# Optimization experiments

Hardware: AMD Instinct MI355X
Metric: run time of the kernel (lower is better)

The kernel has to match this reference:

```python
import jax, jax.numpy as jnp
import numpy as np

C_IN = 256   # c_m
C_H = 32     # outer_product_dim
C_Z = 128
B, S, N = 1, 128, 256  # batch, msa depth, n_res
EPS = 1e-5


def setup_inputs() -> dict:
    key = jax.random.key(0)
    ks = jax.random.split(key, 10)
    msa = jax.random.normal(ks[0], (B, S, N, C_IN), dtype=jnp.float32)
    mask = jax.random.uniform(ks[1], (B, S, N), dtype=jnp.float32)
    ln_w = jnp.ones((C_IN,), jnp.float32)
    ln_b = jnp.zeros((C_IN,), jnp.float32)
    # weights stored [in, out] (torch Linear transposed)
    wl = jax.random.normal(ks[2], (C_IN, C_H), jnp.float32) / np.sqrt(C_IN)
    bl = jnp.zeros((C_H,), jnp.float32)
    wr = jax.random.normal(ks[3], (C_IN, C_H), jnp.float32) / np.sqrt(C_IN)
    br = jnp.zeros((C_H,), jnp.float32)
    wo = jax.random.normal(ks[4], (C_H * C_H, C_Z), jnp.float32) / np.sqrt(C_H * C_H)
    bo = jnp.zeros((C_Z,), jnp.float32)
    return {"msa_representation": msa, "msa_mask": mask, "ln_w": ln_w, "ln_b": ln_b,
            "wl": wl, "bl": bl, "wr": wr, "br": br, "wo": wo, "bo": bo}


def _layer_norm(x, w, b):
    mu = jnp.mean(x, axis=-1, keepdims=True)
    var = jnp.var(x, axis=-1, keepdims=True)
    return (x - mu) * jax.lax.rsqrt(var + EPS) * w + b


def reference(msa_representation, msa_mask, ln_w, ln_b, wl, bl, wr, br, wo, bo):
    x = _layer_norm(msa_representation, ln_w, ln_b)            # [b,s,i,c_in]
    A = x @ wl + bl                                            # [b,s,i,c]
    Bm = x @ wr + br                                           # [b,s,j,d]
    m = msa_mask
    A = A * m[..., None]
    Bm = Bm * m[..., None]
    outer = jnp.einsum('bsic,bsjd->bijcd', A, Bm)              # [b,i,j,c,d]
    norm = jnp.clip(jnp.einsum('bsi,bsj->bij', m, m), 1.0, None)
    mean_val = outer / norm[..., None, None]
    b_, i_, j_ = mean_val.shape[:3]
    mean_val = mean_val.reshape(b_, i_, j_, -1)                # [b,i,j,c*d]
    return mean_val @ wo + bo                                  # [b,i,j,c_z]
```

## Files before the change

kernel.cpp:

```cpp
#include <hip/hip_runtime.h>
#include <hip/hip_bf16.h>
#include <stdint.h>

#define SDEP 128
#define NRES 256
#define CZQ 128

typedef __bf16 v8bf __attribute__((ext_vector_type(8)));
typedef __bf16 v4bf __attribute__((ext_vector_type(4)));
typedef float v16f __attribute__((ext_vector_type(16)));

__device__ __forceinline__ float dpp_wave_sum(float x) {
  float t;
#define STEP(ctrl)                                                         \
  t = __builtin_bit_cast(float, __builtin_amdgcn_update_dpp(               \
          0, __builtin_bit_cast(int, x), ctrl, 0xF, 0xF, true));           \
  x += t;
  STEP(0x111)
  STEP(0x112)
  STEP(0x114)
  STEP(0x118)
  STEP(0x142)
  STEP(0x143)
#undef STEP
  return x;
}
__device__ __forceinline__ float lane63(float x) {
  return __builtin_bit_cast(float,
      __builtin_amdgcn_readlane(__builtin_bit_cast(int, x), 63));
}

__global__ __launch_bounds__(512, 2) void fusedA_kernel(
    const float* __restrict__ msa, const float* __restrict__ lnw,
    const float* __restrict__ lnb, const float* __restrict__ wl,
    const float* __restrict__ wr, const float* __restrict__ mask,
    const float* __restrict__ wo, const float* __restrict__ bl,
    const float* __restrict__ br,
    __bf16* __restrict__ At2, __bf16* __restrict__ Bt2,
    float* __restrict__ rnorm, __bf16* __restrict__ wot4)
{
  __shared__ __bf16 xs[128 * 258];
  __shared__ __bf16 wcs[16384];
  __shared__ __bf16 Ls[8 * 32 * 36];

  const int i = blockIdx.x, t = threadIdx.x;
  const int w = t >> 6, lane = t & 63;
  const int half = lane >> 5, l31 = lane & 31;
  const int sb = w >> 1, nh = w & 1;

  #pragma unroll
  for (int u = 0; u < 32; ++u) {
    int idx = u * 512 + t;
    int j = idx & 7, n = (idx >> 3) & 31, hf = (idx >> 8) & 1;
    int ks = (idx >> 9) & 15, tile = idx >> 13;
    const float* wsrc = tile ? wr : wl;
    wcs[idx] = (__bf16)wsrc[(ks * 16 + hf * 8 + j) * 32 + n];
  }

  const float4 wv4 = ((const float4*)lnw)[lane];
  const float4 bv4 = ((const float4*)lnb)[lane];

  #pragma unroll 8
  for (int r = 0; r < 16; ++r) {
    const int s = sb * 32 + nh * 16 + r;
    float4 x = ((const float4*)(msa + ((size_t)s * 256 + i) * 256))[lane];
    float s1 = dpp_wave_sum(x.x + x.y + x.z + x.w);
    float s2 = dpp_wave_sum(x.x * x.x + x.y * x.y + x.z * x.z + x.w * x.w);
    float mu = lane63(s1) * (1.f / 256.f);
    float var = lane63(s2) * (1.f / 256.f) - mu * mu;
    float rs = rsqrtf(var + 1e-5f);
    v4bf o;
    o[0] = (__bf16)((x.x - mu) * rs * wv4.x + bv4.x);
    o[1] = (__bf16)((x.y - mu) * rs * wv4.y + bv4.y);
    o[2] = (__bf16)((x.z - mu) * rs * wv4.z + bv4.z);
    o[3] = (__bf16)((x.w - mu) * rs * wv4.w + bv4.w);
    *(v4bf*)(xs + s * 258 + lane * 4) = o;
  }
  __syncthreads();

  v16f acc;
  #pragma unroll
  for (int r = 0; r < 16; ++r) acc[r] = 0.f;

  const __bf16* xrow = xs + (sb * 32 + l31) * 258 + half * 8;
  const __bf16* bbase = wcs + nh * 8192 + half * 256 + l31 * 8;
  #pragma unroll
  for (int ks = 0; ks < 16; ++ks) {
    v8bf a = *(const v8bf*)(xrow + ks * 16);
    v8bf b = *(const v8bf*)(bbase + ks * 512);
    acc = __builtin_amdgcn_mfma_f32_32x32x16_bf16(a, b, acc, 0, 0, 0);
  }

  __bf16* Lw = Ls + w * 32 * 36;
  const float bias = (nh ? br : bl)[l31];
  #pragma unroll
  for (int r = 0; r < 16; ++r) {
    int sl = (r & 3) + 8 * (r >> 2) + 4 * half;
    float mv = mask[(sb * 32 + sl) * NRES + i];
    Lw[l31 * 36 + sl] = (__bf16)((acc[r] + bias) * mv);
  }

  __bf16* dst = nh ? Bt2 : At2;
  const int c = lane >> 1, jq = (lane & 1) * 4;
  #pragma unroll
  for (int o = 0; o < 4; ++o) {
    v4bf v = *(const v4bf*)(Lw + c * 36 + o * 8 + jq);
    *(v4bf*)(dst + ((size_t)i * 16 + sb * 4 + o) * 256 + lane * 4) = v;
  }

  if (i < 128) {
    const int b = i * 2 + (t >> 8), col = t & 255;
    float a0 = 0.f;
    #pragma unroll 4
    for (int s = 0; s < SDEP; ++s)
      a0 += mask[s * NRES + b] * mask[s * NRES + col];
    rnorm[b * NRES + col] = 1.f / fmaxf(a0, 1.f);
  } else {
    #pragma unroll
    for (int u = 0; u < 2; ++u) {
      int idx = (i - 128) * 1024 + u * 512 + t;
      int j = idx & 7, lc = (idx >> 3) & 63, kk = (idx >> 9) & 63, zg = idx >> 15;
      int k = kk * 16 + (lc >> 5) * 8 + j;
      int z = zg * 32 + (lc & 31);
      wot4[idx] = (__bf16)wo[k * CZQ + z];
    }
  }
}

__global__ __launch_bounds__(512, 4) void outer_kernel(
    const __bf16* __restrict__ At2, const __bf16* __restrict__ Bt2,
    const float* __restrict__ rnorm, const __bf16* __restrict__ wot4,
    const float* __restrict__ bo, float* __restrict__ out)
{
  __shared__ char smem[74240];
  __bf16* Ps   = (__bf16*)smem;
  __bf16* redb = (__bf16*)(smem + 66048);

  const int tid = threadIdx.x;
  const int w = tid >> 6, lane = tid & 63;
  const int half = lane >> 5, l31 = lane & 31;
  const int bx = blockIdx.x;
  const int by = blockIdx.y;
  const int mh = w >> 2;
  const int nq = w & 3;

  const __bf16* Ap = At2 + ((size_t)(by * 4 + mh * 2)) * 4096 + l31 * 8;
  const __bf16* Bp = Bt2 + ((size_t)(bx * 8 + nq * 2)) * 4096 + l31 * 8;

  v16f acc[2][2];
  #pragma unroll
  for (int a = 0; a < 2; ++a)
    #pragma unroll
    for (int b = 0; b < 2; ++b)
      #pragma unroll
      for (int r = 0; r < 16; ++r) acc[a][b][r] = 0.f;

  #pragma unroll
  for (int ks = 0; ks < 8; ++ks) {
    const int off = (ks * 2 + half) * 256;
    v8bf a0 = *(const v8bf*)(Ap + off);
    v8bf a1 = *(const v8bf*)(Ap + 4096 + off);
    v8bf b0 = *(const v8bf*)(Bp + off);
    v8bf b1 = *(const v8bf*)(Bp + 4096 + off);
    acc[0][0] = __builtin_amdgcn_mfma_f32_32x32x16_bf16(a0, b0, acc[0][0], 0, 0, 0);
    acc[0][1] = __builtin_amdgcn_mfma_f32_32x32x16_bf16(a0, b1, acc[0][1], 0, 0, 0);
    acc[1][0] = __builtin_amdgcn_mfma_f32_32x32x16_bf16(a1, b0, acc[1][0], 0, 0, 0);
    acc[1][1] = __builtin_amdgcn_mfma_f32_32x32x16_bf16(a1, b1, acc[1][1], 0, 0, 0);
  }

  #pragma unroll
  for (int ti = 0; ti < 2; ++ti) {
    #pragma unroll
    for (int tj = 0; tj < 2; ++tj) {
      const int it = mh * 2 + ti, jt = nq * 2 + tj;
      const int p = it * 8 + jt;
      const float rn = rnorm[(by * 4 + it) * NRES + bx * 8 + jt];
      #pragma unroll
      for (int r = 0; r < 16; ++r) {
        int cc = (r & 3) + 8 * (r >> 2) + 4 * half;
        Ps[p * 1032 + cc * 32 + l31] = (__bf16)(acc[ti][tj][r] * rn);
      }
    }
  }

  const int zg = w & 3, kh = w >> 2;
  const __bf16* wp = wot4 + ((size_t)((zg * 64 + kh * 32) * 64) + half * 32 + l31) * 8;
  v8bf wb[8];
  #pragma unroll
  for (int u = 0; u < 8; ++u)
    wb[u] = *(const v8bf*)(wp + u * 512);

  __syncthreads();

  const __bf16* pp = Ps + l31 * 1032 + kh * 512 + half * 8;

  v16f c2;
  #pragma unroll
  for (int r = 0; r < 16; ++r) c2[r] = 0.f;

  #pragma unroll
  for (int g = 0; g < 4; ++g) {
    #pragma unroll
    for (int u = 0; u < 8; ++u) {
      const int kk = g * 8 + u;
      v8bf bb = wb[u];
      if (g < 3) wb[u] = *(const v8bf*)(wp + (kk + 8) * 512);
      v8bf aa = *(const v8bf*)(pp + kk * 16);
      c2 = __builtin_amdgcn_mfma_f32_32x32x16_bf16(aa, bb, c2, 0, 0, 0);
    }
  }

  if (kh == 1) {
    #pragma unroll
    for (int r = 0; r < 16; ++r) {
      int cc = (r & 3) + 8 * (r >> 2) + 4 * half;
      redb[zg * 1024 + cc * 32 + l31] = (__bf16)c2[r];
    }
  }
  __syncthreads();

  if (kh == 0) {
    const float bz = bo[zg * 32 + l31];
    #pragma unroll
    for (int r = 0; r < 16; ++r) {
      int cc = (r & 3) + 8 * (r >> 2) + 4 * half;
      float v = c2[r] + (float)redb[zg * 1024 + cc * 32 + l31] + bz;
      int i = by * 4 + (cc >> 3), j = bx * 8 + (cc & 7);
      out[((size_t)i * NRES + j) * CZQ + zg * 32 + l31] = v;
    }
  }
}

extern "C" void kernel_launch(void* const* d_in, const int* in_sizes, int n_in,
                              void* d_out, int out_size, void* d_ws, size_t ws_size,
                              hipStream_t stream) {
  const float* msa  = (const float*)d_in[0];
  const float* mask = (const float*)d_in[1];
  const float* lnw  = (const float*)d_in[2];
  const float* lnb  = (const float*)d_in[3];
  const float* wl   = (const float*)d_in[4];
  const float* bl   = (const float*)d_in[5];
  const float* wr   = (const float*)d_in[6];
  const float* br   = (const float*)d_in[7];
  const float* wo   = (const float*)d_in[8];
  const float* bo   = (const float*)d_in[9];
  float* out = (float*)d_out;

  char* ws = (char*)d_ws;
  __bf16* At2   = (__bf16*)(ws);
  __bf16* Bt2   = (__bf16*)(ws + 2097152);
  float*  rnorm = (float*)(ws + 4194304);
  __bf16* wot4  = (__bf16*)(ws + 4456448);

  fusedA_kernel<<<256, 512, 0, stream>>>(msa, lnw, lnb, wl, wr, mask, wo,
                                         bl, br, At2, Bt2, rnorm, wot4);
  outer_kernel<<<dim3(32, 64), 512, 0, stream>>>(At2, Bt2, rnorm, wot4, bo, out);
}
```

Measured before the change: 150.3 us.

## Make outer kernel persistent over 8 tiles with software-pipelined double-buffered stages

The outer-product kernel now launches 256 blocks instead of 2048, and each block loops over 8 consecutive j-tiles. Inside each iteration the first GEMM for the next tile is interleaved with the projection GEMM of the current tile, with Ps and redb double-buffered in shared memory. Half of the wo tile stays resident in registers for the whole block. The aim is to hide global-load and MFMA latency and amortize weight loading across tiles. In exchange it uses more registers and shared memory, occupancy drops to 2 blocks per CU, and only 256 blocks may leave CUs idle.

```diff
diff --git a/kernel.cpp b/kernel.cpp
--- a/kernel.cpp
+++ b/kernel.cpp
@@ -29,6 +29,8 @@
   return __builtin_bit_cast(float,
       __builtin_amdgcn_readlane(__builtin_bit_cast(int, x), 63));
 }
+
+#define MFMA32(a, b, c) __builtin_amdgcn_mfma_f32_32x32x16_bf16(a, b, c, 0, 0, 0)
 
 __global__ __launch_bounds__(512, 2) void fusedA_kernel(
     const float* __restrict__ msa, const float* __restrict__ lnw,
@@ -88,7 +90,7 @@
   for (int ks = 0; ks < 16; ++ks) {
     v8bf a = *(const v8bf*)(xrow + ks * 16);
     v8bf b = *(const v8bf*)(bbase + ks * 512);
-    acc = __builtin_amdgcn_mfma_f32_32x32x16_bf16(a, b, acc, 0, 0, 0);
+    acc = MFMA32(a, b, acc);
   }
 
   __bf16* Lw = Ls + w * 32 * 36;
@@ -127,106 +129,172 @@
   }
 }
 
-__global__ __launch_bounds__(512, 4) void outer_kernel(
+__global__ __launch_bounds__(512, 2) void outer_kernel(
     const __bf16* __restrict__ At2, const __bf16* __restrict__ Bt2,
     const float* __restrict__ rnorm, const __bf16* __restrict__ wot4,
     const float* __restrict__ bo, float* __restrict__ out)
 {
-  __shared__ char smem[74240];
-  __bf16* Ps   = (__bf16*)smem;
-  __bf16* redb = (__bf16*)(smem + 66048);
+  __shared__ __bf16 Ps[2][32 * 1032];
+  __shared__ __bf16 redb[2][4 * 1024];
 
   const int tid = threadIdx.x;
   const int w = tid >> 6, lane = tid & 63;
   const int half = lane >> 5, l31 = lane & 31;
-  const int bx = blockIdx.x;
-  const int by = blockIdx.y;
-  const int mh = w >> 2;
-  const int nq = w & 3;
+  const int bid = blockIdx.x;
+  const int by = bid >> 2;
+  const int bxg = (bid & 3) * 8;
+  const int mh = w >> 2, nq = w & 3;
+  const int zg = w & 3, kh = w >> 2;
+
+  const __bf16* wp =
+      wot4 + ((size_t)((zg * 64 + kh * 32) * 64) + half * 32 + l31) * 8;
+  v8bf wbr[16];
+  #pragma unroll
+  for (int u = 0; u < 16; ++u) wbr[u] = *(const v8bf*)(wp + u * 512);
 
   const __bf16* Ap = At2 + ((size_t)(by * 4 + mh * 2)) * 4096 + l31 * 8;
-  const __bf16* Bp = Bt2 + ((size_t)(bx * 8 + nq * 2)) * 4096 + l31 * 8;
 
   v16f acc[2][2];
-  #pragma unroll
-  for (int a = 0; a < 2; ++a)
-    #pragma unroll
-    for (int b = 0; b < 2; ++b)
-      #pragma unroll
-      for (int r = 0; r < 16; ++r) acc[a][b][r] = 0.f;
-
-  #pragma unroll
-  for (int ks = 0; ks < 8; ++ks) {
-    const int off = (ks * 2 + half) * 256;
-    v8bf a0 = *(const v8bf*)(Ap + off);
-    v8bf a1 = *(const v8bf*)(Ap + 4096 + off);
-    v8bf b0 = *(const v8bf*)(Bp + off);
-    v8bf b1 = *(const v8bf*)(Bp + 4096 + off);
-    acc[0][0] = __builtin_amdgcn_mfma_f32_32x32x16_bf16(a0, b0, acc[0][0], 0, 0, 0);
-    acc[0][1] = __builtin_amdgcn_mfma_f32_32x32x16_bf16(a0, b1, acc[0][1], 0, 0, 0);
-    acc[1][0] = __builtin_amdgcn_mfma_f32_32x32x16_bf16(a1, b0, acc[1][0], 0, 0, 0);
-    acc[1][1] = __builtin_amdgcn_mfma_f32_32x32x16_bf16(a1, b1, acc[1][1], 0, 0, 0);
-  }
-
-  #pragma unroll
-  for (int ti = 0; ti < 2; ++ti) {
-    #pragma unroll
-    for (int tj = 0; tj < 2; ++tj) {
-      const int it = mh * 2 + ti, jt = nq * 2 + tj;
-      const int p = it * 8 + jt;
-      const float rn = rnorm[(by * 4 + it) * NRES + bx * 8 + jt];
+
+  {
+    const __bf16* Bp = Bt2 + ((size_t)(bxg * 8 + nq * 2)) * 4096 + l31 * 8;
+    #pragma unroll
+    for (int a = 0; a < 2; ++a)
+      #pragma unroll
+      for (int b = 0; b < 2; ++b)
+        #pragma unroll
+        for (int r = 0; r < 16; ++r) acc[a][b][r] = 0.f;
+    #pragma unroll
+    for (int ks = 0; ks < 8; ++ks) {
+      const int off = (ks * 2 + half) * 256;
+      v8bf a0 = *(const v8bf*)(Ap + off);
+      v8bf a1 = *(const v8bf*)(Ap + 4096 + off);
+      v8bf b0 = *(const v8bf*)(Bp + off);
+      v8bf b1 = *(const v8bf*)(Bp + 4096 + off);
+      acc[0][0] = MFMA32(a0, b0, acc[0][0]);
+      acc[0][1] = MFMA32(a0, b1, acc[0][1]);
+      acc[1][0] = MFMA32(a1, b0, acc[1][0]);
+      acc[1][1] = MFMA32(a1, b1, acc[1][1]);
+    }
+    #pragma unroll
+    for (int ti = 0; ti < 2; ++ti) {
+      #pragma unroll
+      for (int tj = 0; tj < 2; ++tj) {
+        const int it = mh * 2 + ti, jt = nq * 2 + tj;
+        const int p = it * 8 + jt;
+        const float rn = rnorm[(by * 4 + it) * NRES + bxg * 8 + jt];
+        #pragma unroll
+        for (int r = 0; r < 16; ++r) {
+          int cc = (r & 3) + 8 * (r >> 2) + 4 * half;
+          Ps[0][p * 1032 + cc * 32 + l31] = (__bf16)(acc[ti][tj][r] * rn);
+        }
+      }
+    }
+  }
+  __syncthreads();
+
+  const __bf16* pp0 = &Ps[0][l31 * 1032 + kh * 512 + half * 8];
+  const __bf16* pp1 = &Ps[1][l31 * 1032 + kh * 512 + half * 8];
+  const float bz = bo[zg * 32 + l31];
+
+  #pragma unroll 1
+  for (int t = 0; t < 8; ++t) {
+    const int pb = t & 1;
+    const int bxn = (t < 7) ? (bxg + t + 1) : bxg;
+    const __bf16* Bp = Bt2 + ((size_t)(bxn * 8 + nq * 2)) * 4096 + l31 * 8;
+    const __bf16* pp = pb ? pp1 : pp0;
+
+    float rn[2][2];
+    #pragma unroll
+    for (int ti = 0; ti < 2; ++ti)
+      #pragma unroll
+      for (int tj = 0; tj < 2; ++tj)
+        rn[ti][tj] =
+            rnorm[(by * 4 + mh * 2 + ti) * NRES + bxn * 8 + nq * 2 + tj];
+
+    #pragma unroll
+    for (int a = 0; a < 2; ++a)
+      #pragma unroll
+      for (int b = 0; b < 2; ++b)
+        #pragma unroll
+        for (int r = 0; r < 16; ++r) acc[a][b][r] = 0.f;
+
+    v16f c2;
+    #pragma unroll
+    for (int r = 0; r < 16; ++r) c2[r] = 0.f;
+
+    v8bf la[2][4];
+    v8bf ws[8];
+
+    {
+      const int off = half * 256;
+      la[0][0] = *(const v8bf*)(Ap + off);
+      la[0][1] = *(const v8bf*)(Ap + 4096 + off);
+      la[0][2] = *(const v8bf*)(Bp + off);
+      la[0][3] = *(const v8bf*)(Bp + 4096 + off);
+    }
+
+    #pragma unroll
+    for (int kk = 0; kk < 32; ++kk) {
+      v8bf aa = *(const v8bf*)(pp + kk * 16);
+      v8bf bb;
+      if (kk < 16) bb = wbr[kk];
+      else         bb = ws[(kk - 16) & 7];
+      c2 = MFMA32(aa, bb, c2);
+
+      if (kk >= 8 && kk < 24)
+        ws[(kk - 8) & 7] = *(const v8bf*)(wp + (kk + 8) * 512);
+
+      if ((kk & 3) == 0 && kk < 28) {
+        const int g = (kk >> 2) + 1;
+        const int off = (g * 2 + half) * 256;
+        la[g & 1][0] = *(const v8bf*)(Ap + off);
+        la[g & 1][1] = *(const v8bf*)(Ap + 4096 + off);
+        la[g & 1][2] = *(const v8bf*)(Bp + off);
+        la[g & 1][3] = *(const v8bf*)(Bp + 4096 + off);
+      }
+      if ((kk & 3) == 2) {
+        const int g = kk >> 2;
+        v8bf a0 = la[g & 1][0], a1 = la[g & 1][1];
+        v8bf b0 = la[g & 1][2], b1 = la[g & 1][3];
+        acc[0][0] = MFMA32(a0, b0, acc[0][0]);
+        acc[0][1] = MFMA32(a0, b1, acc[0][1]);
+        acc[1][0] = MFMA32(a1, b0, acc[1][0]);
+        acc[1][1] = MFMA32(a1, b1, acc[1][1]);
+      }
+    }
+
+    if (kh == 1) {
       #pragma unroll
       for (int r = 0; r < 16; ++r) {
         int cc = (r & 3) + 8 * (r >> 2) + 4 * half;
-        Ps[p * 1032 + cc * 32 + l31] = (__bf16)(acc[ti][tj][r] * rn);
-      }
-    }
-  }
-
-  const int zg = w & 3, kh = w >> 2;
-  const __bf16* wp = wot4 + ((size_t)((zg * 64 + kh * 32) * 64) + half * 32 + l31) * 8;
-  v8bf wb[8];
-  #pragma unroll
-  for (int u = 0; u < 8; ++u)
-    wb[u] = *(const v8bf*)(wp + u * 512);
-
-  __syncthreads();
-
-  const __bf16* pp = Ps + l31 * 1032 + kh * 512 + half * 8;
-
-  v16f c2;
-  #pragma unroll
-  for (int r = 0; r < 16; ++r) c2[r] = 0.f;
-
-  #pragma unroll
-  for (int g = 0; g < 4; ++g) {
-    #pragma unroll
-    for (int u = 0; u < 8; ++u) {
-      const int kk = g * 8 + u;
-      v8bf bb = wb[u];
-      if (g < 3) wb[u] = *(const v8bf*)(wp + (kk + 8) * 512);
-      v8bf aa = *(const v8bf*)(pp + kk * 16);
-      c2 = __builtin_amdgcn_mfma_f32_32x32x16_bf16(aa, bb, c2, 0, 0, 0);
-    }
-  }
-
-  if (kh == 1) {
-    #pragma unroll
-    for (int r = 0; r < 16; ++r) {
-      int cc = (r & 3) + 8 * (r >> 2) + 4 * half;
-      redb[zg * 1024 + cc * 32 + l31] = (__bf16)c2[r];
-    }
-  }
-  __syncthreads();
-
-  if (kh == 0) {
-    const float bz = bo[zg * 32 + l31];
-    #pragma unroll
-    for (int r = 0; r < 16; ++r) {
-      int cc = (r & 3) + 8 * (r >> 2) + 4 * half;
-      float v = c2[r] + (float)redb[zg * 1024 + cc * 32 + l31] + bz;
-      int i = by * 4 + (cc >> 3), j = bx * 8 + (cc & 7);
-      out[((size_t)i * NRES + j) * CZQ + zg * 32 + l31] = v;
+        redb[pb][zg * 1024 + cc * 32 + l31] = (__bf16)c2[r];
+      }
+    }
+    if (t < 7) {
+      #pragma unroll
+      for (int ti = 0; ti < 2; ++ti) {
+        #pragma unroll
+        for (int tj = 0; tj < 2; ++tj) {
+          const int p = (mh * 2 + ti) * 8 + nq * 2 + tj;
+          #pragma unroll
+          for (int r = 0; r < 16; ++r) {
+            int cc = (r & 3) + 8 * (r >> 2) + 4 * half;
+            Ps[pb ^ 1][p * 1032 + cc * 32 + l31] =
+                (__bf16)(acc[ti][tj][r] * rn[ti][tj]);
+          }
+        }
+      }
+    }
+    __syncthreads();
+    if (kh == 0) {
+      #pragma unroll
+      for (int r = 0; r < 16; ++r) {
+        int cc = (r & 3) + 8 * (r >> 2) + 4 * half;
+        float v = c2[r] + (float)redb[pb][zg * 1024 + cc * 32 + l31] + bz;
+        int i = by * 4 + (cc >> 3), j = (bxg + t) * 8 + (cc & 7);
+        out[((size_t)i * NRES + j) * CZQ + zg * 32 + l31] = v;
+      }
     }
   }
 }
@@ -254,5 +322,5 @@
 
   fusedA_kernel<<<256, 512, 0, stream>>>(msa, lnw, lnb, wl, wr, mask, wo,
                                          bl, br, At2, Bt2, rnorm, wot4);
-  outer_kernel<<<dim3(32, 64), 512, 0, stream>>>(At2, Bt2, rnorm, wot4, bo, out);
-}
+  outer_kernel<<<256, 512, 0, stream>>>(At2, Bt2, rnorm, wot4, bo, out);
+}
```

Measured after the change: 200.6 us. +33.4%, slower.

## Process two j-tiles per outer_kernel block to reuse A and Wo fragments

Applied to the files above, without the earlier changes.

Each outer_kernel block now covers 16 j columns instead of 8, computing two sets of outer-product accumulators that share the same A fragments. The Wo weight fragments loaded from global memory are then reused for both projection GEMMs. This halves the grid and the per-output reloads of A and Wo. In exchange, register use and LDS size per block double (launch bounds drop to 2 blocks), which lowers occupancy.

```diff
diff --git a/kernel.cpp b/kernel.cpp
--- a/kernel.cpp
+++ b/kernel.cpp
@@ -29,6 +29,8 @@
   return __builtin_bit_cast(float,
       __builtin_amdgcn_readlane(__builtin_bit_cast(int, x), 63));
 }
+
+#define MFMA32(a, b, c) __builtin_amdgcn_mfma_f32_32x32x16_bf16(a, b, c, 0, 0, 0)
 
 __global__ __launch_bounds__(512, 2) void fusedA_kernel(
     const float* __restrict__ msa, const float* __restrict__ lnw,
@@ -88,7 +90,7 @@
   for (int ks = 0; ks < 16; ++ks) {
     v8bf a = *(const v8bf*)(xrow + ks * 16);
     v8bf b = *(const v8bf*)(bbase + ks * 512);
-    acc = __builtin_amdgcn_mfma_f32_32x32x16_bf16(a, b, acc, 0, 0, 0);
+    acc = MFMA32(a, b, acc);
   }
 
   __bf16* Lw = Ls + w * 32 * 36;
@@ -127,45 +129,53 @@
   }
 }
 
-__global__ __launch_bounds__(512, 4) void outer_kernel(
+__global__ __launch_bounds__(512, 2) void outer_kernel(
     const __bf16* __restrict__ At2, const __bf16* __restrict__ Bt2,
     const float* __restrict__ rnorm, const __bf16* __restrict__ wot4,
     const float* __restrict__ bo, float* __restrict__ out)
 {
-  __shared__ char smem[74240];
-  __bf16* Ps   = (__bf16*)smem;
-  __bf16* redb = (__bf16*)(smem + 66048);
+  __shared__ __bf16 Ps[2][32 * 1032];
+  __shared__ __bf16 redb[2][4 * 1024];
 
   const int tid = threadIdx.x;
   const int w = tid >> 6, lane = tid & 63;
   const int half = lane >> 5, l31 = lane & 31;
-  const int bx = blockIdx.x;
+  const int bxp = blockIdx.x;
   const int by = blockIdx.y;
   const int mh = w >> 2;
   const int nq = w & 3;
-
-  const __bf16* Ap = At2 + ((size_t)(by * 4 + mh * 2)) * 4096 + l31 * 8;
-  const __bf16* Bp = Bt2 + ((size_t)(bx * 8 + nq * 2)) * 4096 + l31 * 8;
-
-  v16f acc[2][2];
+  const int zg = w & 3;
+  const int kh = w >> 2;
+
+  const __bf16* Ap  = At2 + ((size_t)(by * 4 + mh * 2)) * 4096 + l31 * 8;
+  const __bf16* Bpa = Bt2 + ((size_t)(bxp * 16 + nq * 2)) * 4096 + l31 * 8;
+  const __bf16* Bpb = Bpa + 8 * 4096;
+
+  v16f aca[2][2], acb[2][2];
   #pragma unroll
   for (int a = 0; a < 2; ++a)
     #pragma unroll
     for (int b = 0; b < 2; ++b)
       #pragma unroll
-      for (int r = 0; r < 16; ++r) acc[a][b][r] = 0.f;
+      for (int r = 0; r < 16; ++r) { aca[a][b][r] = 0.f; acb[a][b][r] = 0.f; }
 
   #pragma unroll
   for (int ks = 0; ks < 8; ++ks) {
     const int off = (ks * 2 + half) * 256;
-    v8bf a0 = *(const v8bf*)(Ap + off);
-    v8bf a1 = *(const v8bf*)(Ap + 4096 + off);
-    v8bf b0 = *(const v8bf*)(Bp + off);
-    v8bf b1 = *(const v8bf*)(Bp + 4096 + off);
-    acc[0][0] = __builtin_amdgcn_mfma_f32_32x32x16_bf16(a0, b0, acc[0][0], 0, 0, 0);
-    acc[0][1] = __builtin_amdgcn_mfma_f32_32x32x16_bf16(a0, b1, acc[0][1], 0, 0, 0);
-    acc[1][0] = __builtin_amdgcn_mfma_f32_32x32x16_bf16(a1, b0, acc[1][0], 0, 0, 0);
-    acc[1][1] = __builtin_amdgcn_mfma_f32_32x32x16_bf16(a1, b1, acc[1][1], 0, 0, 0);
+    v8bf a0  = *(const v8bf*)(Ap + off);
+    v8bf a1  = *(const v8bf*)(Ap + 4096 + off);
+    v8bf b0a = *(const v8bf*)(Bpa + off);
+    v8bf b1a = *(const v8bf*)(Bpa + 4096 + off);
+    v8bf b0b = *(const v8bf*)(Bpb + off);
+    v8bf b1b = *(const v8bf*)(Bpb + 4096 + off);
+    aca[0][0] = MFMA32(a0, b0a, aca[0][0]);
+    aca[0][1] = MFMA32(a0, b1a, aca[0][1]);
+    aca[1][0] = MFMA32(a1, b0a, aca[1][0]);
+    aca[1][1] = MFMA32(a1, b1a, aca[1][1]);
+    acb[0][0] = MFMA32(a0, b0b, acb[0][0]);
+    acb[0][1] = MFMA32(a0, b1b, acb[0][1]);
+    acb[1][0] = MFMA32(a1, b0b, acb[1][0]);
+    acb[1][1] = MFMA32(a1, b1b, acb[1][1]);
   }
 
   #pragma unroll
@@ -174,29 +184,33 @@
     for (int tj = 0; tj < 2; ++tj) {
       const int it = mh * 2 + ti, jt = nq * 2 + tj;
       const int p = it * 8 + jt;
-      const float rn = rnorm[(by * 4 + it) * NRES + bx * 8 + jt];
+      const float rna = rnorm[(by * 4 + it) * NRES + bxp * 16 + jt];
+      const float rnb = rnorm[(by * 4 + it) * NRES + bxp * 16 + 8 + jt];
       #pragma unroll
       for (int r = 0; r < 16; ++r) {
         int cc = (r & 3) + 8 * (r >> 2) + 4 * half;
-        Ps[p * 1032 + cc * 32 + l31] = (__bf16)(acc[ti][tj][r] * rn);
+        Ps[0][p * 1032 + cc * 32 + l31] = (__bf16)(aca[ti][tj][r] * rna);
+        Ps[1][p * 1032 + cc * 32 + l31] = (__bf16)(acb[ti][tj][r] * rnb);
       }
     }
   }
 
-  const int zg = w & 3, kh = w >> 2;
-  const __bf16* wp = wot4 + ((size_t)((zg * 64 + kh * 32) * 64) + half * 32 + l31) * 8;
+  const __bf16* wp =
+      wot4 + ((size_t)((zg * 64 + kh * 32) * 64) + half * 32 + l31) * 8;
   v8bf wb[8];
   #pragma unroll
   for (int u = 0; u < 8; ++u)
     wb[u] = *(const v8bf*)(wp + u * 512);
+  const float bz = bo[zg * 32 + l31];
 
   __syncthreads();
 
-  const __bf16* pp = Ps + l31 * 1032 + kh * 512 + half * 8;
-
-  v16f c2;
-  #pragma unroll
-  for (int r = 0; r < 16; ++r) c2[r] = 0.f;
+  const __bf16* ppa = &Ps[0][l31 * 1032 + kh * 512 + half * 8];
+  const __bf16* ppb = &Ps[1][l31 * 1032 + kh * 512 + half * 8];
+
+  v16f c2a, c2b;
+  #pragma unroll
+  for (int r = 0; r < 16; ++r) { c2a[r] = 0.f; c2b[r] = 0.f; }
 
   #pragma unroll
   for (int g = 0; g < 4; ++g) {
@@ -205,8 +219,10 @@
       const int kk = g * 8 + u;
       v8bf bb = wb[u];
       if (g < 3) wb[u] = *(const v8bf*)(wp + (kk + 8) * 512);
-      v8bf aa = *(const v8bf*)(pp + kk * 16);
-      c2 = __builtin_amdgcn_mfma_f32_32x32x16_bf16(aa, bb, c2, 0, 0, 0);
+      v8bf aaa = *(const v8bf*)(ppa + kk * 16);
+      v8bf aab = *(const v8bf*)(ppb + kk * 16);
+      c2a = MFMA32(aaa, bb, c2a);
+      c2b = MFMA32(aab, bb, c2b);
     }
   }
 
@@ -214,19 +230,21 @@
     #pragma unroll
     for (int r = 0; r < 16; ++r) {
       int cc = (r & 3) + 8 * (r >> 2) + 4 * half;
-      redb[zg * 1024 + cc * 32 + l31] = (__bf16)c2[r];
+      redb[0][zg * 1024 + cc * 32 + l31] = (__bf16)c2a[r];
+      redb[1][zg * 1024 + cc * 32 + l31] = (__bf16)c2b[r];
     }
   }
   __syncthreads();
 
   if (kh == 0) {
-    const float bz = bo[zg * 32 + l31];
     #pragma unroll
     for (int r = 0; r < 16; ++r) {
       int cc = (r & 3) + 8 * (r >> 2) + 4 * half;
-      float v = c2[r] + (float)redb[zg * 1024 + cc * 32 + l31] + bz;
-      int i = by * 4 + (cc >> 3), j = bx * 8 + (cc & 7);
-      out[((size_t)i * NRES + j) * CZQ + zg * 32 + l31] = v;
+      int i = by * 4 + (cc >> 3);
+      float va = c2a[r] + (float)redb[0][zg * 1024 + cc * 32 + l31] + bz;
+      float vb = c2b[r] + (float)redb[1][zg * 1024 + cc * 32 + l31] + bz;
+      out[((size_t)i * NRES + bxp * 16 + (cc & 7)) * CZQ + zg * 32 + l31] = va;
+      out[((size_t)i * NRES + bxp * 16 + 8 + (cc & 7)) * CZQ + zg * 32 + l31] = vb;
     }
   }
 }
@@ -254,5 +272,5 @@
 
   fusedA_kernel<<<256, 512, 0, stream>>>(msa, lnw, lnb, wl, wr, mask, wo,
                                          bl, br, At2, Bt2, rnorm, wot4);
-  outer_kernel<<<dim3(32, 64), 512, 0, stream>>>(At2, Bt2, rnorm, wot4, bo, out);
-}
+  outer_kernel<<<dim3(16, 64), 512, 0, stream>>>(At2, Bt2, rnorm, wot4, bo, out);
+}
```

Result: no change. 151.6 us (+0.9%).

## Warp-specialize outer kernel into double-buffered producer/consumer pipeline over j tiles

Applied to the files above, without the earlier changes.

Rewrites the outer-product kernel so each block loops over 8 j-tiles. Four waves compute the A·B outer products into a double-buffered LDS tile while the other four waves run the projection against wo and write output. This removes the split-K reduction through LDS and amortizes weight loads across tiles. It shrinks the grid to 256 blocks, and the stage work is uneven, so the consumer waves may dominate the runtime.

```diff
diff --git a/kernel.cpp b/kernel.cpp
--- a/kernel.cpp
+++ b/kernel.cpp
@@ -5,6 +5,7 @@
 #define SDEP 128
 #define NRES 256
 #define CZQ 128
+#define NT 8
 
 typedef __bf16 v8bf __attribute__((ext_vector_type(8)));
 typedef __bf16 v4bf __attribute__((ext_vector_type(4)));
@@ -29,6 +30,8 @@
   return __builtin_bit_cast(float,
       __builtin_amdgcn_readlane(__builtin_bit_cast(int, x), 63));
 }
+
+#define MFMA32(a, b, c) __builtin_amdgcn_mfma_f32_32x32x16_bf16(a, b, c, 0, 0, 0)
 
 __global__ __launch_bounds__(512, 2) void fusedA_kernel(
     const float* __restrict__ msa, const float* __restrict__ lnw,
@@ -88,7 +91,7 @@
   for (int ks = 0; ks < 16; ++ks) {
     v8bf a = *(const v8bf*)(xrow + ks * 16);
     v8bf b = *(const v8bf*)(bbase + ks * 512);
-    acc = __builtin_amdgcn_mfma_f32_32x32x16_bf16(a, b, acc, 0, 0, 0);
+    acc = MFMA32(a, b, acc);
   }
 
   __bf16* Lw = Ls + w * 32 * 36;
@@ -127,106 +130,124 @@
   }
 }
 
-__global__ __launch_bounds__(512, 4) void outer_kernel(
+__global__ __launch_bounds__(512, 2) void outer_kernel(
     const __bf16* __restrict__ At2, const __bf16* __restrict__ Bt2,
     const float* __restrict__ rnorm, const __bf16* __restrict__ wot4,
     const float* __restrict__ bo, float* __restrict__ out)
 {
-  __shared__ char smem[74240];
-  __bf16* Ps   = (__bf16*)smem;
-  __bf16* redb = (__bf16*)(smem + 66048);
+  __shared__ __bf16 Ps[2][32 * 1032];
 
   const int tid = threadIdx.x;
   const int w = tid >> 6, lane = tid & 63;
   const int half = lane >> 5, l31 = lane & 31;
-  const int bx = blockIdx.x;
+  const int bxq = blockIdx.x;
   const int by = blockIdx.y;
-  const int mh = w >> 2;
-  const int nq = w & 3;
-
-  const __bf16* Ap = At2 + ((size_t)(by * 4 + mh * 2)) * 4096 + l31 * 8;
-  const __bf16* Bp = Bt2 + ((size_t)(bx * 8 + nq * 2)) * 4096 + l31 * 8;
-
-  v16f acc[2][2];
-  #pragma unroll
-  for (int a = 0; a < 2; ++a)
+
+  if (w < 4) {
+    const int mh = w >> 1;
+    const int nh = w & 1;
+    const __bf16* Ap = At2 + ((size_t)(by * 4 + mh * 2)) * 4096 + l31 * 8;
+
+    auto g1tile = [&](int tt) {
+      const int buf = tt & 1;
+      const int jb = bxq * 64 + tt * 8;
+      const __bf16* Bp = Bt2 + ((size_t)(jb + nh * 4)) * 4096 + l31 * 8;
+
+      float rn[2][4];
+      #pragma unroll
+      for (int ti = 0; ti < 2; ++ti)
+        #pragma unroll
+        for (int tj = 0; tj < 4; ++tj)
+          rn[ti][tj] = rnorm[(by * 4 + mh * 2 + ti) * NRES + jb + nh * 4 + tj];
+
+      v16f acc[2][4];
+      #pragma unroll
+      for (int a = 0; a < 2; ++a)
+        #pragma unroll
+        for (int b = 0; b < 4; ++b)
+          #pragma unroll
+          for (int r = 0; r < 16; ++r) acc[a][b][r] = 0.f;
+
+      #pragma unroll
+      for (int ks = 0; ks < 8; ++ks) {
+        const int off = (ks * 2 + half) * 256;
+        v8bf a0 = *(const v8bf*)(Ap + off);
+        v8bf a1 = *(const v8bf*)(Ap + 4096 + off);
+        v8bf b0 = *(const v8bf*)(Bp + off);
+        v8bf b1 = *(const v8bf*)(Bp + 4096 + off);
+        v8bf b2 = *(const v8bf*)(Bp + 8192 + off);
+        v8bf b3 = *(const v8bf*)(Bp + 12288 + off);
+        acc[0][0] = MFMA32(a0, b0, acc[0][0]);
+        acc[0][1] = MFMA32(a0, b1, acc[0][1]);
+        acc[0][2] = MFMA32(a0, b2, acc[0][2]);
+        acc[0][3] = MFMA32(a0, b3, acc[0][3]);
+        acc[1][0] = MFMA32(a1, b0, acc[1][0]);
+        acc[1][1] = MFMA32(a1, b1, acc[1][1]);
+        acc[1][2] = MFMA32(a1, b2, acc[1][2]);
+        acc[1][3] = MFMA32(a1, b3, acc[1][3]);
+      }
+
+      #pragma unroll
+      for (int ti = 0; ti < 2; ++ti) {
+        #pragma unroll
+        for (int tj = 0; tj < 4; ++tj) {
+          const int p = (mh * 2 + ti) * 8 + nh * 4 + tj;
+          #pragma unroll
+          for (int r = 0; r < 16; ++r) {
+            int cc = (r & 3) + 8 * (r >> 2) + 4 * half;
+            Ps[buf][p * 1032 + cc * 32 + l31] =
+                (__bf16)(acc[ti][tj][r] * rn[ti][tj]);
+          }
+        }
+      }
+    };
+
+    g1tile(0);
+    __syncthreads();
+    #pragma unroll 1
+    for (int t = 0; t < NT; ++t) {
+      if (t < NT - 1) g1tile(t + 1);
+      if (t < NT - 1) __syncthreads();
+    }
+  } else {
+    const int zg = w - 4;
+    const __bf16* wp = wot4 + (size_t)zg * 32768 + (half * 32 + l31) * 8;
+    const float bz = bo[zg * 32 + l31];
+
+    v8bf wb[16];
     #pragma unroll
-    for (int b = 0; b < 2; ++b)
-      #pragma unroll
-      for (int r = 0; r < 16; ++r) acc[a][b][r] = 0.f;
-
-  #pragma unroll
-  for (int ks = 0; ks < 8; ++ks) {
-    const int off = (ks * 2 + half) * 256;
-    v8bf a0 = *(const v8bf*)(Ap + off);
-    v8bf a1 = *(const v8bf*)(Ap + 4096 + off);
-    v8bf b0 = *(const v8bf*)(Bp + off);
-    v8bf b1 = *(const v8bf*)(Bp + 4096 + off);
-    acc[0][0] = __builtin_amdgcn_mfma_f32_32x32x16_bf16(a0, b0, acc[0][0], 0, 0, 0);
-    acc[0][1] = __builtin_amdgcn_mfma_f32_32x32x16_bf16(a0, b1, acc[0][1], 0, 0, 0);
-    acc[1][0] = __builtin_amdgcn_mfma_f32_32x32x16_bf16(a1, b0, acc[1][0], 0, 0, 0);
-    acc[1][1] = __builtin_amdgcn_mfma_f32_32x32x16_bf16(a1, b1, acc[1][1], 0, 0, 0);
-  }
-
-  #pragma unroll
-  for (int ti = 0; ti < 2; ++ti) {
-    #pragma unroll
-    for (int tj = 0; tj < 2; ++tj) {
-      const int it = mh * 2 + ti, jt = nq * 2 + tj;
-      const int p = it * 8 + jt;
-      const float rn = rnorm[(by * 4 + it) * NRES + bx * 8 + jt];
+    for (int u = 0; u < 16; ++u) wb[u] = *(const v8bf*)(wp + u * 512);
+
+    __syncthreads();
+    #pragma unroll 1
+    for (int t = 0; t < NT; ++t) {
+      const __bf16* pp = &Ps[t & 1][l31 * 1032 + half * 8];
+
+      v16f c20, c21;
+      #pragma unroll
+      for (int r = 0; r < 16; ++r) { c20[r] = 0.f; c21[r] = 0.f; }
+
+      v8bf ws[16];
+      #pragma unroll
+      for (int kk = 0; kk < 64; ++kk) {
+        v8bf aa = *(const v8bf*)(pp + kk * 16);
+        v8bf bb = (kk < 16) ? wb[kk] : ws[kk & 15];
+        if (kk & 1) c21 = MFMA32(aa, bb, c21);
+        else        c20 = MFMA32(aa, bb, c20);
+        if (kk < 48)
+          ws[kk & 15] = *(const v8bf*)(wp + (kk + 16) * 512);
+      }
+
       #pragma unroll
       for (int r = 0; r < 16; ++r) {
         int cc = (r & 3) + 8 * (r >> 2) + 4 * half;
-        Ps[p * 1032 + cc * 32 + l31] = (__bf16)(acc[ti][tj][r] * rn);
-      }
-    }
-  }
-
-  const int zg = w & 3, kh = w >> 2;
-  const __bf16* wp = wot4 + ((size_t)((zg * 64 + kh * 32) * 64) + half * 32 + l31) * 8;
-  v8bf wb[8];
-  #pragma unroll
-  for (int u = 0; u < 8; ++u)
-    wb[u] = *(const v8bf*)(wp + u * 512);
-
-  __syncthreads();
-
-  const __bf16* pp = Ps + l31 * 1032 + kh * 512 + half * 8;
-
-  v16f c2;
-  #pragma unroll
-  for (int r = 0; r < 16; ++r) c2[r] = 0.f;
-
-  #pragma unroll
-  for (int g = 0; g < 4; ++g) {
-    #pragma unroll
-    for (int u = 0; u < 8; ++u) {
-      const int kk = g * 8 + u;
-      v8bf bb = wb[u];
-      if (g < 3) wb[u] = *(const v8bf*)(wp + (kk + 8) * 512);
-      v8bf aa = *(const v8bf*)(pp + kk * 16);
-      c2 = __builtin_amdgcn_mfma_f32_32x32x16_bf16(aa, bb, c2, 0, 0, 0);
-    }
-  }
-
-  if (kh == 1) {
-    #pragma unroll
-    for (int r = 0; r < 16; ++r) {
-      int cc = (r & 3) + 8 * (r >> 2) + 4 * half;
-      redb[zg * 1024 + cc * 32 + l31] = (__bf16)c2[r];
-    }
-  }
-  __syncthreads();
-
-  if (kh == 0) {
-    const float bz = bo[zg * 32 + l31];
-    #pragma unroll
-    for (int r = 0; r < 16; ++r) {
-      int cc = (r & 3) + 8 * (r >> 2) + 4 * half;
-      float v = c2[r] + (float)redb[zg * 1024 + cc * 32 + l31] + bz;
-      int i = by * 4 + (cc >> 3), j = bx * 8 + (cc & 7);
-      out[((size_t)i * NRES + j) * CZQ + zg * 32 + l31] = v;
+        int i = by * 4 + (cc >> 3);
+        int j = bxq * 64 + t * 8 + (cc & 7);
+        out[((size_t)i * NRES + j) * CZQ + zg * 32 + l31] =
+            c20[r] + c21[r] + bz;
+      }
+
+      if (t < NT - 1) __syncthreads();
     }
   }
 }
@@ -254,5 +275,5 @@
 
   fusedA_kernel<<<256, 512, 0, stream>>>(msa, lnw, lnb, wl, wr, mask, wo,
                                          bl, br, At2, Bt2, rnorm, wot4);
-  outer_kernel<<<dim3(32, 64), 512, 0, stream>>>(At2, Bt2, rnorm, wot4, bo, out);
-}
+  outer_kernel<<<dim3(4, 64), 512, 0, stream>>>(At2, Bt2, rnorm, wot4, bo, out);
+}
```

Result: slower. 167.0 us (+11.1%).
